# Optimization experiments

Measured on AMD Instinct MI355X. Metric: run time of the kernel, lower is better.

Reference implementation:

```python
import jax, jax.numpy as jnp
import numpy as np

N_NODES = 100_000
N_EDGES = 500_000
G = 1024          # num_graphs
H = 128           # hidden_dim
S_PER = 4         # start nodes per graph
EPS_LN = 1e-5


def _ln(x, g, b):
    m = x.mean(-1, keepdims=True)
    v = ((x - m) ** 2).mean(-1, keepdims=True)
    return (x - m) / jnp.sqrt(v + EPS_LN) * g + b


def _gelu(x):
    return jax.nn.gelu(x, approximate=False)  # torch nn.GELU default (erf)


def setup_inputs() -> dict:
    key = jax.random.key(0)
    ks = jax.random.split(key, 24)
    S = G * S_PER
    d = {
        'node_tokens': jax.random.normal(ks[0], (N_NODES, H), jnp.float32),
        'question_tokens': jax.random.normal(ks[1], (G, H), jnp.float32),
        'edge_tokens': jax.random.normal(ks[2], (N_EDGES, H), jnp.float32),
        'start_node_locals': jax.random.randint(ks[3], (S,), 0, N_NODES),
        'start_node_ptr': jnp.arange(G + 1) * S_PER,
        'edge_batch': jnp.sort(jax.random.randint(ks[4], (N_EDGES,), 0, G)),
        'selected_mask': jax.random.bernoulli(ks[5], 0.5, (N_EDGES,)),
        'edge_index': jax.random.randint(ks[6], (2, N_EDGES), 0, N_NODES),
    }
    w = lambda k, shp: jax.random.normal(k, shp, jnp.float32) * 0.02
    # log_z_head: LN(H) -> Linear(H,H) -> GELU -> Linear(H,1)
    d['ln1_g'] = jnp.ones((H,)); d['ln1_b'] = jnp.zeros((H,))
    d['zw1'] = w(ks[7], (H, H)); d['zb1'] = w(ks[8], (H,))
    d['zw2'] = w(ks[9], (H, 1)); d['zb2'] = jnp.zeros((1,))
    # ctx_projector: Linear(2H,H) -> GELU -> Linear(H,H)
    d['cw1'] = w(ks[10], (2 * H, H)); d['cb1'] = w(ks[11], (H,))
    d['cw2'] = w(ks[12], (H, H)); d['cb2'] = w(ks[13], (H,))
    # backward_head: LN(3H) -> Linear(3H,H) -> GELU -> (Dropout: identity in eval) -> Linear(H,1)
    d['bln_g'] = jnp.ones((3 * H,)); d['bln_b'] = jnp.zeros((3 * H,))
    d['bw1'] = w(ks[14], (3 * H, H)); d['bb1'] = w(ks[15], (H,))
    d['bw2'] = w(ks[16], (H, 1)); d['bb2'] = jnp.zeros((1,))
    return d


def reference(node_tokens, question_tokens, edge_tokens,
              ln1_g, ln1_b, zw1, zb1, zw2, zb2,
              cw1, cb1, cw2, cb2,
              bln_g, bln_b, bw1, bb1, bw2, bb2,
              start_node_locals, start_node_ptr, edge_batch, selected_mask, edge_index):
    counts = start_node_ptr[1:] - start_node_ptr[:-1]                       # [G]
    batch_index = jnp.repeat(jnp.arange(G), counts, total_repeat_length=start_node_locals.shape[0])
    # --- aggregate_start: gather + segment softmax + scatter-add ---
    start_tokens = node_tokens[start_node_locals]                            # [S,H]
    q = question_tokens[batch_index]                                         # [S,H]
    scores = (start_tokens * q).sum(-1) / jnp.sqrt(jnp.float32(H))           # [S]
    m = jax.ops.segment_max(scores, batch_index, num_segments=G)             # [G]
    ex = jnp.exp(scores - m[batch_index])
    denom = jax.ops.segment_sum(ex, batch_index, num_segments=G)
    alpha = ex / denom[batch_index]                                          # pyg_softmax (eps-free path)
    summary = jax.ops.segment_sum(start_tokens * alpha[:, None], batch_index, num_segments=G)  # [G,H]
    # --- build_context + log_z ---
    ctx_in = jnp.concatenate([summary, question_tokens], axis=-1)            # [G,2H]
    context = _gelu(ctx_in @ cw1 + cb1) @ cw2 + cb2                          # [G,H]
    log_z = (_gelu(_ln(context, ln1_g, ln1_b) @ zw1 + zb1) @ zw2 + zb2)[:, 0]  # [G]
    # --- log_pb (learned): gather + segment log-softmax over target nodes + scatter-add per graph ---
    tgt = edge_index[1]                                                      # [E]
    tail = node_tokens[tgt]                                                  # [E,H]
    edge_ctx = jnp.concatenate([edge_tokens, question_tokens[edge_batch], tail], axis=-1)  # [E,3H]
    logits = (_gelu(_ln(edge_ctx, bln_g, bln_b) @ bw1 + bb1) @ bw2 + bb2)[:, 0]            # [E]
    tmax = jax.ops.segment_max(logits, tgt, num_segments=N_NODES)
    shifted = logits - tmax[tgt]
    lse = jnp.log(jax.ops.segment_sum(jnp.exp(shifted), tgt, num_segments=N_NODES))
    log_probs = shifted - lse[tgt]                                           # scatter_log_softmax
    sel = selected_mask.astype(logits.dtype)
    log_pb_per_graph = jax.ops.segment_sum(log_probs * sel, edge_batch, num_segments=G)    # [G]
    # pb_nll: masked mean over graphs that have a selected edge
    nll_per_graph = jax.ops.segment_sum(-log_probs * sel, edge_batch, num_segments=G)
    has_edge = jax.ops.segment_sum(sel, edge_batch, num_segments=G) > 0
    pb_nll = jnp.where(has_edge, nll_per_graph, 0.0).sum() / jnp.maximum(has_edge.sum(), 1).astype(logits.dtype)
    return jnp.stack([log_z, log_pb_per_graph, jnp.broadcast_to(pb_nll, log_z.shape)], axis=-1)  # [G,3]
```

## Files before the change

### kernel.cpp

```cpp
#include <hip/hip_runtime.h>
#include <math.h>

#define G_NUM 1024
#define H 128
#define NNODES 100000
#define NEDGES 500000
#define EPS_LN 1e-5f

typedef __attribute__((ext_vector_type(8))) short short8;
typedef __attribute__((ext_vector_type(4))) float f32x4;

__device__ __forceinline__ float gelu_exact(float x) {
    return 0.5f * x * (1.0f + erff(x * 0.70710678118654752440f));
}
__device__ __forceinline__ unsigned short f2bf(float x) {
    unsigned u = __float_as_uint(x);
    return (unsigned short)((u + 0x7FFFu + ((u >> 16) & 1u)) >> 16);
}

__global__ void k_probe_mask(const unsigned* __restrict__ mw, int* __restrict__ flag) {
    unsigned v = mw[threadIdx.x];
    if (v == 0x3F800000u) atomicOr(flag, 2);
    else if (v > 1u) atomicOr(flag, 1);
}

__global__ void k_prep(const float* __restrict__ bw1, const float* __restrict__ blng,
                       unsigned short* __restrict__ bwbf) {
    int e = blockIdx.x * 256 + threadIdx.x;
    if (e >= 384 * 128) return;
    int k = e >> 7, n = e & 127;
    int s = k >> 5, krel = k & 31;
    int quad = krel >> 3, j = krel & 7;
    int lane = quad * 16 + (n & 15);
    int t8 = n >> 4;
    bwbf[((s * 8 + t8) * 64 + lane) * 8 + j] = f2bf(bw1[e] * blng[k]);
}

__global__ __launch_bounds__(128) void k_prep2(const float* __restrict__ bw1,
                                               const float* __restrict__ blng,
                                               const float* __restrict__ blnb,
                                               const float* __restrict__ bb1,
                                               float* __restrict__ colsum,
                                               float* __restrict__ bb1p) {
    int n = threadIdx.x;
    float cs = 0.f, bs = 0.f;
    for (int k = 0; k < 384; ++k) {
        float w = bw1[k * H + n];
        cs += blng[k] * w;
        bs += blnb[k] * w;
    }
    colsum[n] = cs;
    bb1p[n] = bb1[n] + bs;
}

__global__ __launch_bounds__(128) void k_graph(
    const float* __restrict__ node_tokens, const float* __restrict__ question,
    const int* __restrict__ locals_, const int* __restrict__ ptr,
    const float* __restrict__ cw1, const float* __restrict__ cb1,
    const float* __restrict__ cw2, const float* __restrict__ cb2,
    const float* __restrict__ ln1g, const float* __restrict__ ln1b,
    const float* __restrict__ zw1, const float* __restrict__ zb1,
    const float* __restrict__ zw2, const float* __restrict__ zb2,
    float* __restrict__ out)
{
    int g = blockIdx.x, t = threadIdx.x;
    __shared__ float xin[2 * H];
    __shared__ float buf[H];
    __shared__ float r1[2], r2[2];
    __shared__ float sc[16];
    int p0 = ptr[g], p1 = ptr[g + 1];
    int cnt = p1 - p0; if (cnt > 16) cnt = 16;
    float q = question[(size_t)g * H + t];
    xin[H + t] = q;
    for (int s = 0; s < cnt; ++s) {
        int node = locals_[p0 + s];
        float v = node_tokens[(size_t)node * H + t] * q;
        for (int off = 32; off; off >>= 1) v += __shfl_down(v, off);
        if ((t & 63) == 0) r1[t >> 6] = v;
        __syncthreads();
        if (t == 0) sc[s] = (r1[0] + r1[1]) * 0.08838834764831845f;
        __syncthreads();
    }
    float m = -1e30f;
    for (int s = 0; s < cnt; ++s) m = fmaxf(m, sc[s]);
    float den = 0.f;
    for (int s = 0; s < cnt; ++s) den += expf(sc[s] - m);
    float acc0 = 0.f;
    for (int s = 0; s < cnt; ++s) {
        float a = expf(sc[s] - m) / den;
        acc0 += a * node_tokens[(size_t)locals_[p0 + s] * H + t];
    }
    xin[t] = acc0;
    __syncthreads();
    float a1 = cb1[t];
    for (int k = 0; k < 2 * H; ++k) a1 += xin[k] * cw1[k * H + t];
    buf[t] = gelu_exact(a1);
    __syncthreads();
    float ctx = cb2[t];
    for (int k = 0; k < H; ++k) ctx += buf[k] * cw2[k * H + t];
    float s1 = ctx, s2 = ctx * ctx;
    for (int off = 32; off; off >>= 1) { s1 += __shfl_down(s1, off); s2 += __shfl_down(s2, off); }
    if ((t & 63) == 0) { r1[t >> 6] = s1; r2[t >> 6] = s2; }
    __syncthreads();
    float mean = (r1[0] + r1[1]) * (1.f / H);
    float var  = (r2[0] + r2[1]) * (1.f / H) - mean * mean;
    float xn = (ctx - mean) * rsqrtf(var + EPS_LN) * ln1g[t] + ln1b[t];
    __syncthreads();
    buf[t] = xn;
    __syncthreads();
    float a2 = zb1[t];
    for (int k = 0; k < H; ++k) a2 += buf[k] * zw1[k * H + t];
    float p = gelu_exact(a2) * zw2[t];
    for (int off = 32; off; off >>= 1) p += __shfl_down(p, off);
    if ((t & 63) == 0) r1[t >> 6] = p;
    __syncthreads();
    if (t == 0) out[(size_t)g * 3 + 0] = r1[0] + r1[1] + zb2[0];
}

__global__ __launch_bounds__(256) void k_edges(
    const float* __restrict__ node_tokens, const float* __restrict__ question,
    const float* __restrict__ edge_tokens, const int* __restrict__ edge_batch,
    const int* __restrict__ edge_index,
    const unsigned short* __restrict__ bwbf, const float* __restrict__ colsum,
    const float* __restrict__ bb1p, const float* __restrict__ bw2,
    const float* __restrict__ bb2, float* __restrict__ logits,
    float* __restrict__ sumexp)
{
    int t = threadIdx.x, lane = t & 63, w = t >> 6;
    int quad = lane >> 4, n16 = lane & 15;
    const int* tgt_idx = edge_index + NEDGES;

    int e0w = blockIdx.x * 128 + w * 32;
    int ea = e0w + n16;       int eca = ea < NEDGES ? ea : NEDGES - 1;
    int eb = e0w + 16 + n16;  int ecb = eb < NEDGES ? eb : NEDGES - 1;
    int qra = edge_batch[eca], qrb = edge_batch[ecb];
    int tra = tgt_idx[eca],    trb = tgt_idx[ecb];
    const float4* epa = (const float4*)(edge_tokens + (size_t)eca * H);
    const float4* qpa = (const float4*)(question + (size_t)qra * H);
    const float4* npa = (const float4*)(node_tokens + (size_t)tra * H);
    const float4* epb = (const float4*)(edge_tokens + (size_t)ecb * H);
    const float4* qpb = (const float4*)(question + (size_t)qrb * H);
    const float4* npb = (const float4*)(node_tokens + (size_t)trb * H);

    float s1a = 0.f, s2a = 0.f, s1b = 0.f, s2b = 0.f;
    f32x4 acc0[8], acc1[8];
    #pragma unroll
    for (int i = 0; i < 8; ++i) { acc0[i] = (f32x4){0,0,0,0}; acc1[i] = (f32x4){0,0,0,0}; }

    #pragma unroll
    for (int s = 0; s < 12; ++s) {
        int c0 = s * 8 + quad * 2;
        int cc = c0 - ((s < 4) ? 0 : (s < 8) ? 32 : 64);
        const float4* basea = (s < 4) ? epa : (s < 8) ? qpa : npa;
        const float4* baseb = (s < 4) ? epb : (s < 8) ? qpb : npb;
        float4 v0 = basea[cc], v1 = basea[cc + 1];
        float4 u0 = baseb[cc], u1 = baseb[cc + 1];
        s1a += v0.x + v0.y + v0.z + v0.w + v1.x + v1.y + v1.z + v1.w;
        s2a += v0.x*v0.x + v0.y*v0.y + v0.z*v0.z + v0.w*v0.w
             + v1.x*v1.x + v1.y*v1.y + v1.z*v1.z + v1.w*v1.w;
        s1b += u0.x + u0.y + u0.z + u0.w + u1.x + u1.y + u1.z + u1.w;
        s2b += u0.x*u0.x + u0.y*u0.y + u0.z*u0.z + u0.w*u0.w
             + u1.x*u1.x + u1.y*u1.y + u1.z*u1.z + u1.w*u1.w;
        short8 fa, fb;
        fa[0] = (short)f2bf(v0.x); fa[1] = (short)f2bf(v0.y);
        fa[2] = (short)f2bf(v0.z); fa[3] = (short)f2bf(v0.w);
        fa[4] = (short)f2bf(v1.x); fa[5] = (short)f2bf(v1.y);
        fa[6] = (short)f2bf(v1.z); fa[7] = (short)f2bf(v1.w);
        fb[0] = (short)f2bf(u0.x); fb[1] = (short)f2bf(u0.y);
        fb[2] = (short)f2bf(u0.z); fb[3] = (short)f2bf(u0.w);
        fb[4] = (short)f2bf(u1.x); fb[5] = (short)f2bf(u1.y);
        fb[6] = (short)f2bf(u1.z); fb[7] = (short)f2bf(u1.w);
        #pragma unroll
        for (int t8 = 0; t8 < 8; ++t8) {
            short8 b = *(const short8*)&bwbf[((s * 8 + t8) * 64 + lane) * 8];
            acc0[t8] = __builtin_amdgcn_mfma_f32_16x16x32_bf16(fa, b, acc0[t8], 0, 0, 0);
            acc1[t8] = __builtin_amdgcn_mfma_f32_16x16x32_bf16(fb, b, acc1[t8], 0, 0, 0);
        }
    }

    s1a += __shfl_xor(s1a, 16); s1a += __shfl_xor(s1a, 32);
    s2a += __shfl_xor(s2a, 16); s2a += __shfl_xor(s2a, 32);
    s1b += __shfl_xor(s1b, 16); s1b += __shfl_xor(s1b, 32);
    s2b += __shfl_xor(s2b, 16); s2b += __shfl_xor(s2b, 32);
    float mua  = s1a * (1.f / 384.f);
    float inva = rsqrtf(s2a * (1.f / 384.f) - mua * mua + EPS_LN);
    float mub  = s1b * (1.f / 384.f);
    float invb = rsqrtf(s2b * (1.f / 384.f) - mub * mub + EPS_LN);
    float bb2v = bb2[0];

    #pragma unroll
    for (int h = 0; h < 2; ++h) {
        float muh  = h ? mub : mua;
        float invh = h ? invb : inva;
        #pragma unroll
        for (int r = 0; r < 4; ++r) {
            float mu_r  = __shfl(muh,  quad * 4 + r);
            float inv_r = __shfl(invh, quad * 4 + r);
            float ssum = 0.f;
            #pragma unroll
            for (int t8 = 0; t8 < 8; ++t8) {
                int n = t8 * 16 + n16;
                float a = h ? acc1[t8][r] : acc0[t8][r];
                float y = (a - mu_r * colsum[n]) * inv_r + bb1p[n];
                ssum += gelu_exact(y) * bw2[n];
            }
            ssum += __shfl_xor(ssum, 1);
            ssum += __shfl_xor(ssum, 2);
            ssum += __shfl_xor(ssum, 4);
            ssum += __shfl_xor(ssum, 8);
            if (n16 == 0) {
                int ei = e0w + h * 16 + quad * 4 + r;
                if (ei < NEDGES) {
                    float lg = ssum + bb2v;
                    logits[ei] = lg;
                    atomicAdd(&sumexp[tgt_idx[ei]], expf(lg));
                }
            }
        }
    }
}

__global__ __launch_bounds__(256) void k_logpb(
    const float* __restrict__ logits,
    const int* __restrict__ edge_index,
    const int* __restrict__ edge_batch,
    const void* __restrict__ mask,
    const int* __restrict__ flag,
    const float* __restrict__ sumexp,
    float* __restrict__ logpb, int* __restrict__ selcnt)
{
    __shared__ float lacc[8];
    __shared__ int lcnt[8];
    __shared__ int g0s, big;
    int t = threadIdx.x;
    int e0 = blockIdx.x * 256;
    if (t == 0) {
        int ga = edge_batch[e0 < NEDGES ? e0 : NEDGES - 1];
        int el = e0 + 255; if (el >= NEDGES) el = NEDGES - 1;
        int gb = edge_batch[el];
        g0s = ga; big = (gb - ga > 7);
    }
    if (t < 8) { lacc[t] = 0.f; lcnt[t] = 0; }
    __syncthreads();
    int e = e0 + t;
    if (e < NEDGES) {
        int mode = *flag;
        bool sel;
        if (mode & 2)      sel = ((const float*)mask)[e] != 0.f;
        else if (mode & 1) sel = ((const unsigned char*)mask)[e] != 0;
        else               sel = ((const int*)mask)[e] != 0;
        if (sel) {
            int tg = edge_index[NEDGES + e];
            float lp = logits[e] - logf(sumexp[tg]);
            int g = edge_batch[e];
            if (!big) {
                atomicAdd(&lacc[g - g0s], lp);
                atomicAdd(&lcnt[g - g0s], 1);
            } else {
                atomicAdd(&logpb[g], lp);
                atomicAdd(&selcnt[g], 1);
            }
        }
    }
    __syncthreads();
    if (t < 8 && !big && lcnt[t] > 0) {
        atomicAdd(&logpb[g0s + t], lacc[t]);
        atomicAdd(&selcnt[g0s + t], lcnt[t]);
    }
}

__global__ __launch_bounds__(1024) void k_final(const float* __restrict__ logpb,
                                                const int* __restrict__ selcnt,
                                                float* __restrict__ out)
{
    int g = threadIdx.x;
    float lpb = logpb[g];
    int has = selcnt[g] > 0;
    float s = has ? -lpb : 0.f;
    int c = has;
    __shared__ float rn[16];
    __shared__ int rh[16];
    __shared__ float pbnll_s;
    for (int off = 32; off; off >>= 1) { s += __shfl_down(s, off); c += __shfl_down(c, off); }
    if ((g & 63) == 0) { rn[g >> 6] = s; rh[g >> 6] = c; }
    __syncthreads();
    if (g == 0) {
        float ts = 0.f; int tc = 0;
        for (int i = 0; i < 16; ++i) { ts += rn[i]; tc += rh[i]; }
        pbnll_s = ts / (float)(tc > 0 ? tc : 1);
    }
    __syncthreads();
    out[(size_t)g * 3 + 1] = lpb;
    out[(size_t)g * 3 + 2] = pbnll_s;
}

extern "C" void kernel_launch(void* const* d_in, const int* in_sizes, int n_in,
                              void* d_out, int out_size, void* d_ws, size_t ws_size,
                              hipStream_t stream) {
    const float* node_tokens = (const float*)d_in[0];
    const float* question    = (const float*)d_in[1];
    const float* edge_tokens = (const float*)d_in[2];
    const int*   locals_     = (const int*)d_in[3];
    const int*   ptr         = (const int*)d_in[4];
    const int*   edge_batch  = (const int*)d_in[5];
    const void*  mask        = d_in[6];
    const int*   edge_index  = (const int*)d_in[7];
    const float* ln1g = (const float*)d_in[8];
    const float* ln1b = (const float*)d_in[9];
    const float* zw1  = (const float*)d_in[10];
    const float* zb1  = (const float*)d_in[11];
    const float* zw2  = (const float*)d_in[12];
    const float* zb2  = (const float*)d_in[13];
    const float* cw1  = (const float*)d_in[14];
    const float* cb1  = (const float*)d_in[15];
    const float* cw2  = (const float*)d_in[16];
    const float* cb2  = (const float*)d_in[17];
    const float* blng = (const float*)d_in[18];
    const float* blnb = (const float*)d_in[19];
    const float* bw1  = (const float*)d_in[20];
    const float* bb1  = (const float*)d_in[21];
    const float* bw2  = (const float*)d_in[22];
    const float* bb2  = (const float*)d_in[23];
    float* out = (float*)d_out;

    float* ws = (float*)d_ws;
    float* sumexp  = ws;
    float* logpb   = ws + 100000;
    int*   selcnt  = (int*)(ws + 101024);
    int*   flag    = (int*)(ws + 102048);
    float* logits  = ws + 102052;
    float* colsum  = ws + 602052;
    float* bb1p    = ws + 602180;
    unsigned short* bwbf = (unsigned short*)(ws + 602308);

    hipMemsetAsync(d_ws, 0, (size_t)102049 * 4, stream);
    k_probe_mask<<<1, 256, 0, stream>>>((const unsigned*)mask, flag);
    k_prep<<<192, 256, 0, stream>>>(bw1, blng, bwbf);
    k_prep2<<<1, 128, 0, stream>>>(bw1, blng, blnb, bb1, colsum, bb1p);
    k_graph<<<G_NUM, 128, 0, stream>>>(node_tokens, question, locals_, ptr,
                                       cw1, cb1, cw2, cb2, ln1g, ln1b,
                                       zw1, zb1, zw2, zb2, out);
    k_edges<<<(NEDGES + 127) / 128, 256, 0, stream>>>(node_tokens, question, edge_tokens,
                                                      edge_batch, edge_index, bwbf,
                                                      colsum, bb1p, bw2, bb2,
                                                      logits, sumexp);
    int eb = (NEDGES + 255) / 256;
    k_logpb<<<eb, 256, 0, stream>>>(logits, edge_index, edge_batch, mask, flag,
                                    sumexp, logpb, selcnt);
    k_final<<<1, 1024, 0, stream>>>(logpb, selcnt, out);
}
```

Before: 730.6 us.

## Stage bf16 weights through double-buffered LDS and merge prep kernels

```diff
diff --git a/kernel.cpp b/kernel.cpp
--- a/kernel.cpp
+++ b/kernel.cpp
@@ -18,39 +18,46 @@
     return (unsigned short)((u + 0x7FFFu + ((u >> 16) & 1u)) >> 16);
 }
 
-__global__ void k_probe_mask(const unsigned* __restrict__ mw, int* __restrict__ flag) {
-    unsigned v = mw[threadIdx.x];
-    if (v == 0x3F800000u) atomicOr(flag, 2);
-    else if (v > 1u) atomicOr(flag, 1);
-}
-
-__global__ void k_prep(const float* __restrict__ bw1, const float* __restrict__ blng,
-                       unsigned short* __restrict__ bwbf) {
-    int e = blockIdx.x * 256 + threadIdx.x;
-    if (e >= 384 * 128) return;
-    int k = e >> 7, n = e & 127;
-    int s = k >> 5, krel = k & 31;
-    int quad = krel >> 3, j = krel & 7;
-    int lane = quad * 16 + (n & 15);
-    int t8 = n >> 4;
-    bwbf[((s * 8 + t8) * 64 + lane) * 8 + j] = f2bf(bw1[e] * blng[k]);
-}
-
-__global__ __launch_bounds__(128) void k_prep2(const float* __restrict__ bw1,
-                                               const float* __restrict__ blng,
-                                               const float* __restrict__ blnb,
-                                               const float* __restrict__ bb1,
-                                               float* __restrict__ colsum,
-                                               float* __restrict__ bb1p) {
-    int n = threadIdx.x;
-    float cs = 0.f, bs = 0.f;
-    for (int k = 0; k < 384; ++k) {
-        float w = bw1[k * H + n];
-        cs += blng[k] * w;
-        bs += blnb[k] * w;
-    }
-    colsum[n] = cs;
-    bb1p[n] = bb1[n] + bs;
+__global__ __launch_bounds__(256) void k_prep_all(
+    const float* __restrict__ bw1, const float* __restrict__ blng,
+    const float* __restrict__ blnb, const float* __restrict__ bb1,
+    unsigned short* __restrict__ bwbf, float* __restrict__ colsum,
+    float* __restrict__ bb1p,
+    const unsigned* __restrict__ mw, int* __restrict__ flag)
+{
+    __shared__ float rc[4], rb[4];
+    int b = blockIdx.x, t = threadIdx.x;
+    if (b < 192) {
+        int e = b * 256 + t;
+        int k = e >> 7, n = e & 127;
+        int s = k >> 5, krel = k & 31;
+        int quad = krel >> 3, j = krel & 7;
+        int lane = quad * 16 + (n & 15);
+        int t8 = n >> 4;
+        bwbf[((s * 8 + t8) * 64 + lane) * 8 + j] = f2bf(bw1[e] * blng[k]);
+    } else if (b < 320) {
+        int n = b - 192;
+        float cs = 0.f, bs = 0.f;
+        for (int k = t; k < 384; k += 256) {
+            float w = bw1[k * H + n];
+            cs += blng[k] * w;
+            bs += blnb[k] * w;
+        }
+        for (int off = 32; off; off >>= 1) {
+            cs += __shfl_down(cs, off);
+            bs += __shfl_down(bs, off);
+        }
+        if ((t & 63) == 0) { rc[t >> 6] = cs; rb[t >> 6] = bs; }
+        __syncthreads();
+        if (t == 0) {
+            colsum[n] = rc[0] + rc[1] + rc[2] + rc[3];
+            bb1p[n]   = bb1[n] + rb[0] + rb[1] + rb[2] + rb[3];
+        }
+    } else {
+        unsigned v = mw[t];
+        if (v == 0x3F800000u) atomicOr(flag, 2);
+        else if (v > 1u) atomicOr(flag, 1);
+    }
 }
 
 __global__ __launch_bounds__(128) void k_graph(
@@ -126,6 +133,7 @@
     const float* __restrict__ bb2, float* __restrict__ logits,
     float* __restrict__ sumexp)
 {
+    __shared__ unsigned short bstage[2][4096];
     int t = threadIdx.x, lane = t & 63, w = t >> 6;
     int quad = lane >> 4, n16 = lane & 15;
     const int* tgt_idx = edge_index + NEDGES;
@@ -142,6 +150,14 @@
     const float4* qpb = (const float4*)(question + (size_t)qrb * H);
     const float4* npb = (const float4*)(node_tokens + (size_t)trb * H);
 
+    {
+        const uint4* src = (const uint4*)bwbf;
+        uint4 p0 = src[t], p1 = src[t + 256];
+        uint4* dst = (uint4*)bstage[0];
+        dst[t] = p0; dst[t + 256] = p1;
+    }
+    __syncthreads();
+
     float s1a = 0.f, s2a = 0.f, s1b = 0.f, s2b = 0.f;
     f32x4 acc0[8], acc1[8];
     #pragma unroll
@@ -149,6 +165,12 @@
 
     #pragma unroll
     for (int s = 0; s < 12; ++s) {
+        int cur = s & 1;
+        uint4 p0, p1;
+        if (s < 11) {
+            const uint4* src = (const uint4*)(bwbf + (s + 1) * 4096);
+            p0 = src[t]; p1 = src[t + 256];
+        }
         int c0 = s * 8 + quad * 2;
         int cc = c0 - ((s < 4) ? 0 : (s < 8) ? 32 : 64);
         const float4* basea = (s < 4) ? epa : (s < 8) ? qpa : npa;
@@ -172,9 +194,14 @@
         fb[6] = (short)f2bf(u1.z); fb[7] = (short)f2bf(u1.w);
         #pragma unroll
         for (int t8 = 0; t8 < 8; ++t8) {
-            short8 b = *(const short8*)&bwbf[((s * 8 + t8) * 64 + lane) * 8];
+            short8 b = *(const short8*)&bstage[cur][(t8 * 64 + lane) * 8];
             acc0[t8] = __builtin_amdgcn_mfma_f32_16x16x32_bf16(fa, b, acc0[t8], 0, 0, 0);
             acc1[t8] = __builtin_amdgcn_mfma_f32_16x16x32_bf16(fb, b, acc1[t8], 0, 0, 0);
+        }
+        if (s < 11) {
+            uint4* dst = (uint4*)bstage[cur ^ 1];
+            dst[t] = p0; dst[t + 256] = p1;
+            __syncthreads();
         }
     }
 
@@ -334,9 +361,8 @@
     unsigned short* bwbf = (unsigned short*)(ws + 602308);
 
     hipMemsetAsync(d_ws, 0, (size_t)102049 * 4, stream);
-    k_probe_mask<<<1, 256, 0, stream>>>((const unsigned*)mask, flag);
-    k_prep<<<192, 256, 0, stream>>>(bw1, blng, bwbf);
-    k_prep2<<<1, 128, 0, stream>>>(bw1, blng, blnb, bb1, colsum, bb1p);
+    k_prep_all<<<321, 256, 0, stream>>>(bw1, blng, blnb, bb1, bwbf, colsum, bb1p,
+                                        (const unsigned*)mask, flag);
     k_graph<<<G_NUM, 128, 0, stream>>>(node_tokens, question, locals_, ptr,
                                        cw1, cb1, cw2, cb2, ln1g, ln1b,
                                        zw1, zb1, zw2, zb2, out);
```

Result: faster. 697.6 us (-4.5%).
